# Kernel optimization log

Measured on AMD Instinct MI355X. Metric: run time of the kernel, lower is better.

## Reference

```python
import jax, jax.numpy as jnp
import numpy as np

B, S, H, E, V = 128, 128, 1024, 512, 32000

def setup_inputs() -> dict:
    key = jax.random.key(0)
    ks = jax.random.split(key, 14)
    sc = 0.02
    return {
        "x": jax.random.randint(ks[0], (B,), 0, V),
        "hidden": jax.random.normal(ks[1], (1, B, H), jnp.float32),
        "cell": jax.random.normal(ks[2], (1, B, H), jnp.float32),
        "encoder_outputs": jax.random.normal(ks[3], (B, S, H), jnp.float32),
        # parameters
        "emb_table": jax.random.normal(ks[4], (V, E), jnp.float32) * sc,
        "attn_W": jax.random.normal(ks[5], (H, 2 * H), jnp.float32) * sc,
        "attn_b": jnp.zeros((H,), jnp.float32),
        "v": jax.random.uniform(ks[6], (H,), jnp.float32),
        "W_ih": jax.random.normal(ks[7], (4 * H, E + H), jnp.float32) * sc,
        "W_hh": jax.random.normal(ks[8], (4 * H, H), jnp.float32) * sc,
        "b_ih": jnp.zeros((4 * H,), jnp.float32),
        "b_hh": jnp.zeros((4 * H,), jnp.float32),
        "fc_W": jax.random.normal(ks[9], (V, 2 * H), jnp.float32) * sc,
        "fc_b": jnp.zeros((V,), jnp.float32),
    }


def reference(x, hidden, cell, encoder_outputs, emb_table, attn_W, attn_b, v,
              W_ih, W_hh, b_ih, b_hh, fc_W, fc_b):
    b, s, h = encoder_outputs.shape
    h_last = hidden[-1]                      # [B,H]
    c_last = cell[-1]                        # [B,H]

    # Bahdanau attention
    h_rep = jnp.broadcast_to(h_last[:, None, :], (b, s, h))          # [B,S,H]
    cat = jnp.concatenate([h_rep, encoder_outputs], axis=2)          # [B,S,2H]
    energy = jnp.tanh(jnp.einsum('bsk,hk->bsh', cat, attn_W) + attn_b)
    score = jnp.einsum('bsh,h->bs', energy, v)                       # [B,S]
    attn_weights = jax.nn.softmax(score, axis=1)                     # [B,S]
    context = jnp.einsum('bs,bsh->bh', attn_weights, encoder_outputs)  # [B,H]

    # LSTM single step, gate order i,f,g,o (PyTorch convention)
    emb = emb_table[x]                                               # [B,E]
    xin = jnp.concatenate([emb, context], axis=1)                    # [B,E+H]
    gates = xin @ W_ih.T + b_ih + h_last @ W_hh.T + b_hh             # [B,4H]
    i, f, g, o = jnp.split(gates, 4, axis=1)
    c_new = jax.nn.sigmoid(f) * c_last + jax.nn.sigmoid(i) * jnp.tanh(g)
    h_new = jax.nn.sigmoid(o) * jnp.tanh(c_new)

    out = jnp.concatenate([h_new, context], axis=1)                  # [B,2H]
    logits = out @ fc_W.T + fc_b                                     # [B,V]
    return logits, h_new[None], c_new[None], attn_weights
```

## Files before the change

### kernel.cpp

```cpp
#include <hip/hip_runtime.h>
#include <hip/hip_bf16.h>
#include <math.h>

constexpr int B  = 128;
constexpr int S  = 128;
constexpr int H  = 1024;
constexpr int E  = 512;
constexpr int V  = 32000;
constexpr int H2 = 2 * H;
constexpr int G4 = 4 * H;
constexpr int KX = E + H;
constexpr int KG = KX + H;
constexpr int BS = B * S;
constexpr int KSPLIT = 4;
constexpr int KSEG = KG / KSPLIT;
constexpr int QSPLIT = 4;
constexpr int QSEG = H / QSPLIT;

typedef float  f32x4  __attribute__((ext_vector_type(4)));
typedef short  short8 __attribute__((ext_vector_type(8)));

#define VMCNT(N) asm volatile("s_waitcnt vmcnt(" #N ")" ::: "memory")
#define SBAR     asm volatile("s_barrier" ::: "memory")
#define SCHED0   __builtin_amdgcn_sched_barrier(0)

__device__ __forceinline__ short f2bf(float f) {
    union { float f; unsigned u; } x; x.f = f;
    unsigned r = (x.u + 0x7FFFu + ((x.u >> 16) & 1u)) >> 16;
    return (short)r;
}
__device__ __forceinline__ float bf2f(unsigned short u) {
    union { unsigned u; float f; } x; x.u = ((unsigned)u) << 16;
    return x.f;
}
__device__ __forceinline__ float fast_tanh(float x) {
    float z = fminf(fmaxf(x, -15.f), 15.f);
    float e = __expf(2.f * z);
    return 1.f - __fdividef(2.f, e + 1.f);
}
__device__ __forceinline__ short8 cvt8(float4 a, float4 b) {
    short8 r;
    r[0] = f2bf(a.x); r[1] = f2bf(a.y); r[2] = f2bf(a.z); r[3] = f2bf(a.w);
    r[4] = f2bf(b.x); r[5] = f2bf(b.y); r[6] = f2bf(b.z); r[7] = f2bf(b.w);
    return r;
}
__device__ __forceinline__ void glds16(const void* g, void* l) {
    __builtin_amdgcn_global_load_lds(
        (const __attribute__((address_space(1))) unsigned int*)g,
        (__attribute__((address_space(3))) unsigned int*)l,
        16, 0, 0);
}

__global__ __launch_bounds__(256) void k_pre(const float* __restrict__ enc,
                                             short* __restrict__ encb,
                                             const float* __restrict__ attn_W,
                                             short* __restrict__ w2b) {
    int bid = blockIdx.x;
    if (bid < 16384) {
        size_t p = (size_t)bid * 256 + threadIdx.x;
        float4 a = *(const float4*)(enc + p * 4);
        short4 o = { f2bf(a.x), f2bf(a.y), f2bf(a.z), f2bf(a.w) };
        *(short4*)(encb + p * 4) = o;
    } else {
        int p = (bid - 16384) * 256 + threadIdx.x;
        int row = p >> 8;
        int c = (p & 255) * 4;
        float4 a = *(const float4*)(attn_W + (size_t)row * H2 + H + c);
        short4 o = { f2bf(a.x), f2bf(a.y), f2bf(a.z), f2bf(a.w) };
        *(short4*)(w2b + (size_t)row * H + c) = o;
    }
}

__global__ __launch_bounds__(256) void k_q_mfma(const float* __restrict__ hlast,
                                                const float* __restrict__ attn_W,
                                                float* __restrict__ qpart) {
    __shared__ __align__(16) float A_s[2 * 4096];
    __shared__ __align__(16) float B_s[2 * 1024];

    const int tid  = threadIdx.x;
    const int wave = tid >> 6, lane = tid & 63;
    const int c16 = lane & 15, q4 = lane >> 4;
    const int n0 = blockIdx.x * 32;
    const int kbeg = blockIdx.y * QSEG;

    const int sc = ((lane & 7) ^ ((lane >> 3) & 7)) * 4;
    const int rA = (lane >> 3);
    const int rowB = wave * 8 + (lane >> 3);

    const float* gB = attn_W + (size_t)(n0 + rowB) * H2 + sc;

    auto stage = [&](int k0, int abo, int bbo) {
#pragma unroll
        for (int j = 0; j < 4; j++) {
            int row = wave * 32 + j * 8 + rA;
            glds16(hlast + (size_t)row * H + k0 + sc,
                   A_s + abo + wave * 1024 + j * 256);
        }
        glds16(gB + k0, B_s + bbo + wave * 256);
    };

    f32x4 acc[2][2] = {};
    stage(kbeg, 0, 0);

    for (int kk = 0; kk < QSEG / 32; kk++) {
        const int abo = (kk & 1) << 12;
        const int bbo = (kk & 1) << 10;
        if (kk < QSEG / 32 - 1) {
            stage(kbeg + (kk + 1) * 32, abo ^ 4096, bbo ^ 1024);
            VMCNT(5);
        } else {
            VMCNT(0);
        }
        SCHED0; SBAR;

        short8 a[2], bfr[2];
#pragma unroll
        for (int i = 0; i < 2; i++) {
            int ar = wave * 32 + i * 16 + c16;
            int cl = (2 * q4) ^ (ar & 7);
            float4 lo = *(const float4*)(A_s + abo + ar * 32 + cl * 4);
            float4 hi = *(const float4*)(A_s + abo + ar * 32 + (cl ^ 1) * 4);
            a[i] = cvt8(lo, hi);
        }
#pragma unroll
        for (int j = 0; j < 2; j++) {
            int rb = j * 16 + c16;
            int cl = (2 * q4) ^ (rb & 7);
            float4 lo = *(const float4*)(B_s + bbo + rb * 32 + cl * 4);
            float4 hi = *(const float4*)(B_s + bbo + rb * 32 + (cl ^ 1) * 4);
            bfr[j] = cvt8(lo, hi);
        }
#pragma unroll
        for (int i = 0; i < 2; i++)
#pragma unroll
            for (int j = 0; j < 2; j++)
                acc[i][j] = __builtin_amdgcn_mfma_f32_16x16x32_bf16(a[i], bfr[j], acc[i][j], 0, 0, 0);

        SCHED0; SBAR;
    }

    float* qp = qpart + (size_t)blockIdx.y * B * H;
#pragma unroll
    for (int i = 0; i < 2; i++)
#pragma unroll
        for (int j = 0; j < 2; j++)
#pragma unroll
            for (int r = 0; r < 4; r++) {
                int R = wave * 32 + i * 16 + q4 * 4 + r;
                int n = n0 + j * 16 + c16;
                qp[(size_t)R * H + n] = acc[i][j][r];
            }
}

__global__ __launch_bounds__(256) void k_energy_mfma(const short* __restrict__ encb,
                                                     const short* __restrict__ w2b,
                                                     const float* __restrict__ qpart,
                                                     const float* __restrict__ attn_b,
                                                     const float* __restrict__ v,
                                                     float* __restrict__ part) {
    __shared__ __align__(16) char smem[32768];
    short* Af = (short*)smem;
    short* Bf = (short*)(smem + 16384);
    float (*red)[33] = (float(*)[33])smem;

    const int tid  = threadIdx.x;
    const int wave = tid >> 6, lane = tid & 63;
    const int wr = wave >> 1, wc = wave & 1;
    const int c16 = lane & 15, q4 = lane >> 4;
    const int m0 = blockIdx.x * 128;
    const int n0 = blockIdx.y * 128;

    f32x4 acc[4][4] = {};

    const int scA   = ((lane & 3) ^ ((lane >> 3) & 3)) * 8;
    const int rowA0 = wave * 32 + (lane >> 2);
    const int rowA1 = rowA0 + 16;
    const int sa    = (c16 >> 1) & 3;

    const short* gA = encb + (size_t)m0 * H;
    const short* gB = w2b + (size_t)n0 * H;

    auto stage = [&](int k0, int dst) {
        glds16(gA + (size_t)rowA0 * H + k0 + scA, Af + dst + wave * 1024);
        glds16(gA + (size_t)rowA1 * H + k0 + scA, Af + dst + wave * 1024 + 512);
        glds16(gB + (size_t)rowA0 * H + k0 + scA, Bf + dst + wave * 1024);
        glds16(gB + (size_t)rowA1 * H + k0 + scA, Bf + dst + wave * 1024 + 512);
    };

    stage(0, 0);

    for (int kk = 0; kk < 32; kk++) {
        const int bo = (kk & 1) << 12;
        if (kk < 31) {
            stage((kk + 1) * 32, bo ^ 4096);
            VMCNT(4);
        } else {
            VMCNT(0);
        }
        SCHED0; SBAR;

        short8 a[4], b[4];
#pragma unroll
        for (int i = 0; i < 4; i++) {
            int r = wr * 64 + i * 16 + c16;
            a[i] = *(const short8*)(Af + bo + r * 32 + (q4 ^ sa) * 8);
        }
#pragma unroll
        for (int j = 0; j < 4; j++) {
            int r = wc * 64 + j * 16 + c16;
            b[j] = *(const short8*)(Bf + bo + r * 32 + (q4 ^ sa) * 8);
        }
#pragma unroll
        for (int i = 0; i < 4; i++)
#pragma unroll
            for (int j = 0; j < 4; j++)
                acc[i][j] = __builtin_amdgcn_mfma_f32_16x16x32_bf16(a[i], b[j], acc[i][j], 0, 0, 0);

        SCHED0; SBAR;
    }

    const int bb = blockIdx.x;
    float qv[4], vv[4];
#pragma unroll
    for (int j = 0; j < 4; j++) {
        int n = n0 + wc * 64 + j * 16 + c16;
        float s = attn_b[n];
#pragma unroll
        for (int kh = 0; kh < QSPLIT; kh++)
            s += qpart[((size_t)kh * B + bb) * H + n];
        qv[j] = s;
        vv[j] = v[n];
    }

#pragma unroll
    for (int i = 0; i < 4; i++) {
#pragma unroll
        for (int r = 0; r < 4; r++) {
            float s = 0.f;
#pragma unroll
            for (int j = 0; j < 4; j++)
                s += vv[j] * fast_tanh(qv[j] + acc[i][j][r]);
            red[wr * 64 + i * 16 + q4 * 4 + r][wc * 16 + c16] = s;
        }
    }
    __syncthreads();
    if (tid < 128) {
        float s = 0.f;
#pragma unroll
        for (int c = 0; c < 32; c++) s += red[tid][c];
        part[(size_t)(m0 + tid) * 8 + blockIdx.y] = s;
    }
}

__global__ __launch_bounds__(256) void k_softmax_ctx(const float* __restrict__ part,
                                                     const short* __restrict__ encb,
                                                     const int* __restrict__ x,
                                                     const float* __restrict__ emb,
                                                     const float* __restrict__ hlast,
                                                     float* __restrict__ attn_out,
                                                     short* __restrict__ xinb) {
    const int bid = blockIdx.x;
    const int b = bid >> 2, ch = bid & 3;
    const int tid = threadIdx.x;
    __shared__ float w[S];
    __shared__ float red[128];

    float val = 0.f;
    if (tid < S) {
        const float* p = part + (size_t)(b * S + tid) * 8;
#pragma unroll
        for (int t = 0; t < 8; t++) val += p[t];
        w[tid] = val;
        red[tid] = val;
    }
    __syncthreads();
#pragma unroll
    for (int s = 64; s > 0; s >>= 1) {
        if (tid < s) red[tid] = fmaxf(red[tid], red[tid + s]);
        __syncthreads();
    }
    float m = red[0];
    __syncthreads();
    if (tid < S) { val = __expf(w[tid] - m); red[tid] = val; }
    __syncthreads();
#pragma unroll
    for (int s = 64; s > 0; s >>= 1) {
        if (tid < s) red[tid] += red[tid + s];
        __syncthreads();
    }
    float inv = 1.f / red[0];
    if (tid < S) {
        val *= inv;
        w[tid] = val;
        if (ch == 0) attn_out[b * S + tid] = val;
    }
    if (ch == 1) {
        int xv = x[b];
        float2 e2 = *(const float2*)(emb + (size_t)xv * E + tid * 2);
        short2 eo = { f2bf(e2.x), f2bf(e2.y) };
        *(short2*)(xinb + (size_t)b * KG + tid * 2) = eo;
    } else if (ch == 2) {
        float4 h4 = *(const float4*)(hlast + (size_t)b * H + tid * 4);
        short4 ho = { f2bf(h4.x), f2bf(h4.y), f2bf(h4.z), f2bf(h4.w) };
        *(short4*)(xinb + (size_t)b * KG + KX + tid * 4) = ho;
    }
    __syncthreads();

    const int h = ch * 256 + tid;
    const unsigned short* e = (const unsigned short*)encb + (size_t)b * S * H + h;
    float a0 = 0.f;
#pragma unroll 8
    for (int s = 0; s < S; s++) a0 += w[s] * bf2f(e[(size_t)s * H]);
    xinb[(size_t)b * KG + E + h] = f2bf(a0);
}

__global__ __launch_bounds__(256) void k_gates_mfma(const short* __restrict__ xinb,
                                                    const float* __restrict__ W_ih,
                                                    const float* __restrict__ W_hh,
                                                    float* __restrict__ gpart) {
    __shared__ __align__(16) short A_s[2 * 4096];
    __shared__ __align__(16) float B_s[2 * 1024];

    const int tid  = threadIdx.x;
    const int wave = tid >> 6, lane = tid & 63;
    const int c16 = lane & 15, q4 = lane >> 4;
    const int n0 = blockIdx.x * 32;
    const int kbeg = blockIdx.y * KSEG;

    const int scA   = ((lane & 3) ^ ((lane >> 3) & 3)) * 8;
    const int rowA0 = wave * 32 + (lane >> 2);
    const int rowA1 = rowA0 + 16;
    const int rowB  = wave * 8 + (lane >> 3);
    const int scB   = ((lane & 7) ^ ((lane >> 3) & 7)) * 4;
    const int sa = (c16 >> 1) & 3;
    const int sb = c16 & 7;

    const short* gA0 = xinb + (size_t)rowA0 * KG + scA;
    const short* gA1 = xinb + (size_t)rowA1 * KG + scA;
    const int nr = n0 + rowB;

    auto bsrc = [&](int k0) -> const float* {
        return (k0 < KX) ? (W_ih + (size_t)nr * KX + k0 + scB)
                         : (W_hh + (size_t)nr * H + (k0 - KX) + scB);
    };
    auto stage = [&](int k0, int abo, int bbo) {
        glds16(gA0 + k0, A_s + abo + wave * 1024);
        glds16(gA1 + k0, A_s + abo + wave * 1024 + 512);
        glds16(bsrc(k0), B_s + bbo + wave * 256);
    };

    f32x4 acc[2][2] = {};
    stage(kbeg, 0, 0);

    for (int kk = 0; kk < KSEG / 32; kk++) {
        const int abo = (kk & 1) << 12;
        const int bbo = (kk & 1) << 10;
        if (kk < KSEG / 32 - 1) {
            stage(kbeg + (kk + 1) * 32, abo ^ 4096, bbo ^ 1024);
            VMCNT(3);
        } else {
            VMCNT(0);
        }
        SCHED0; SBAR;

        short8 a[2], bfr[2];
#pragma unroll
        for (int i = 0; i < 2; i++) {
            int r = wave * 32 + i * 16 + c16;
            a[i] = *(const short8*)(A_s + abo + r * 32 + (q4 ^ sa) * 8);
        }
#pragma unroll
        for (int j = 0; j < 2; j++) {
            int rb = j * 16 + c16;
            int cl = (2 * q4) ^ sb;
            float4 lo = *(const float4*)(B_s + bbo + rb * 32 + cl * 4);
            float4 hi = *(const float4*)(B_s + bbo + rb * 32 + (cl ^ 1) * 4);
            bfr[j] = cvt8(lo, hi);
        }
#pragma unroll
        for (int i = 0; i < 2; i++)
#pragma unroll
            for (int j = 0; j < 2; j++)
                acc[i][j] = __builtin_amdgcn_mfma_f32_16x16x32_bf16(a[i], bfr[j], acc[i][j], 0, 0, 0);

        SCHED0; SBAR;
    }

    float* gp = gpart + (size_t)blockIdx.y * B * G4;
#pragma unroll
    for (int i = 0; i < 2; i++)
#pragma unroll
        for (int j = 0; j < 2; j++)
#pragma unroll
            for (int r = 0; r < 4; r++) {
                int R = wave * 32 + i * 16 + q4 * 4 + r;
                int n = n0 + j * 16 + c16;
                gp[(size_t)R * G4 + n] = acc[i][j][r];
            }
}

__global__ __launch_bounds__(256) void k_lstm(const float* __restrict__ gpart,
                                              const float* __restrict__ cell,
                                              const float* __restrict__ b_ih,
                                              const float* __restrict__ b_hh,
                                              const short* __restrict__ xinb,
                                              float* __restrict__ out_h,
                                              float* __restrict__ out_c,
                                              short* __restrict__ xoutb) {
    int idx = blockIdx.x * 256 + threadIdx.x;
    int b = idx >> 10;
    int h = idx & (H - 1);
    float ig = b_ih[h]         + b_hh[h];
    float fg = b_ih[H + h]     + b_hh[H + h];
    float gg = b_ih[2 * H + h] + b_hh[2 * H + h];
    float og = b_ih[3 * H + h] + b_hh[3 * H + h];
#pragma unroll
    for (int p = 0; p < KSPLIT; p++) {
        const float* g = gpart + ((size_t)p * B + b) * G4;
        ig += g[h]; fg += g[H + h]; gg += g[2 * H + h]; og += g[3 * H + h];
    }
    float si = 1.f / (1.f + expf(-ig));
    float sf = 1.f / (1.f + expf(-fg));
    float so = 1.f / (1.f + expf(-og));
    float c = sf * cell[idx] + si * tanhf(gg);
    float hn = so * tanhf(c);
    out_h[idx] = hn;
    out_c[idx] = c;
    xoutb[(size_t)b * H2 + h] = f2bf(hn);
    xoutb[(size_t)b * H2 + H + h] = xinb[(size_t)b * KG + E + h];
}

__global__ __launch_bounds__(256) void k_fc_mfma(const short* __restrict__ xoutb,
                                                 const float* __restrict__ fcW,
                                                 const float* __restrict__ fcb,
                                                 float* __restrict__ logits) {
    __shared__ __align__(16) short A_s[2 * 4096];
    __shared__ __align__(16) float B_s[2 * 1024];

    const int tid  = threadIdx.x;
    const int wave = tid >> 6, lane = tid & 63;
    const int c16 = lane & 15, q4 = lane >> 4;
    const int n0 = blockIdx.x * 32;

    const int scA   = ((lane & 3) ^ ((lane >> 3) & 3)) * 8;
    const int rowA0 = wave * 32 + (lane >> 2);
    const int rowA1 = rowA0 + 16;
    const int rowB  = wave * 8 + (lane >> 3);
    const int scB   = ((lane & 7) ^ ((lane >> 3) & 7)) * 4;
    const int sa = (c16 >> 1) & 3;
    const int sb = c16 & 7;

    const short* gA0 = xoutb + (size_t)rowA0 * H2 + scA;
    const short* gA1 = xoutb + (size_t)rowA1 * H2 + scA;
    const float* gBr = fcW + (size_t)(n0 + rowB) * H2 + scB;

    auto stage = [&](int k0, int abo, int bbo) {
        glds16(gA0 + k0, A_s + abo + wave * 1024);
        glds16(gA1 + k0, A_s + abo + wave * 1024 + 512);
        glds16(gBr + k0, B_s + bbo + wave * 256);
    };

    f32x4 acc[2][2] = {};
    stage(0, 0, 0);

    for (int kk = 0; kk < H2 / 32; kk++) {
        const int abo = (kk & 1) << 12;
        const int bbo = (kk & 1) << 10;
        if (kk < H2 / 32 - 1) {
            stage((kk + 1) * 32, abo ^ 4096, bbo ^ 1024);
            VMCNT(3);
        } else {
            VMCNT(0);
        }
        SCHED0; SBAR;

        short8 a[2], bfr[2];
#pragma unroll
        for (int i = 0; i < 2; i++) {
            int r = wave * 32 + i * 16 + c16;
            a[i] = *(const short8*)(A_s + abo + r * 32 + (q4 ^ sa) * 8);
        }
#pragma unroll
        for (int j = 0; j < 2; j++) {
            int rb = j * 16 + c16;
            int cl = (2 * q4) ^ sb;
            float4 lo = *(const float4*)(B_s + bbo + rb * 32 + cl * 4);
            float4 hi = *(const float4*)(B_s + bbo + rb * 32 + (cl ^ 1) * 4);
            bfr[j] = cvt8(lo, hi);
        }
#pragma unroll
        for (int i = 0; i < 2; i++)
#pragma unroll
            for (int j = 0; j < 2; j++)
                acc[i][j] = __builtin_amdgcn_mfma_f32_16x16x32_bf16(a[i], bfr[j], acc[i][j], 0, 0, 0);

        SCHED0; SBAR;
    }

#pragma unroll
    for (int i = 0; i < 2; i++)
#pragma unroll
        for (int j = 0; j < 2; j++) {
            int n = n0 + j * 16 + c16;
            float bias = fcb[n];
#pragma unroll
            for (int r = 0; r < 4; r++) {
                int R = wave * 32 + i * 16 + q4 * 4 + r;
                logits[(size_t)R * V + n] = acc[i][j][r] + bias;
            }
        }
}

extern "C" void kernel_launch(void* const* d_in, const int* in_sizes, int n_in,
                              void* d_out, int out_size, void* d_ws, size_t ws_size,
                              hipStream_t stream) {
    const int*   x      = (const int*)d_in[0];
    const float* hidden = (const float*)d_in[1];
    const float* cell   = (const float*)d_in[2];
    const float* enc    = (const float*)d_in[3];
    const float* emb    = (const float*)d_in[4];
    const float* attn_W = (const float*)d_in[5];
    const float* attn_b = (const float*)d_in[6];
    const float* v      = (const float*)d_in[7];
    const float* W_ih   = (const float*)d_in[8];
    const float* W_hh   = (const float*)d_in[9];
    const float* b_ih   = (const float*)d_in[10];
    const float* b_hh   = (const float*)d_in[11];
    const float* fc_W   = (const float*)d_in[12];
    const float* fc_b   = (const float*)d_in[13];

    float* out = (float*)d_out;
    float* logits   = out;
    float* out_h    = out + (size_t)B * V;
    float* out_c    = out_h + (size_t)B * H;
    float* out_attn = out_c + (size_t)B * H;

    char* ws = (char*)d_ws;
    short* encb  = (short*)ws;   ws += (size_t)BS * H * 2;
    short* w2b   = (short*)ws;   ws += (size_t)H * H * 2;
    short* xinb  = (short*)ws;   ws += (size_t)B * KG * 2;
    short* xoutb = (short*)ws;   ws += (size_t)B * H2 * 2;
    float* qpart = (float*)ws;   ws += (size_t)QSPLIT * B * H * 4;
    float* part  = (float*)ws;   ws += (size_t)BS * 8 * 4;
    float* gpart = (float*)ws;   ws += (size_t)KSPLIT * B * G4 * 4;

    k_q_mfma<<<dim3(H / 32, QSPLIT), dim3(256), 0, stream>>>(hidden, attn_W, qpart);
    k_pre<<<dim3(16384 + 1024), dim3(256), 0, stream>>>(enc, encb, attn_W, w2b);
    k_energy_mfma<<<dim3(BS / 128, H / 128), dim3(256), 0, stream>>>(encb, w2b, qpart,
                                                                     attn_b, v, part);
    k_softmax_ctx<<<dim3(B * 4), dim3(256), 0, stream>>>(part, encb, x, emb, hidden, out_attn, xinb);
    k_gates_mfma<<<dim3(G4 / 32, KSPLIT), dim3(256), 0, stream>>>(xinb, W_ih, W_hh, gpart);
    k_lstm<<<dim3(B * H / 256), dim3(256), 0, stream>>>(gpart, cell, b_ih, b_hh, xinb,
                                                        out_h, out_c, xoutb);
    k_fc_mfma<<<dim3(V / 32), dim3(256), 0, stream>>>(xoutb, fc_W, fc_b, logits);
}
```

Measured before the change: 580.9 us.

## Deepen global-to-LDS prefetch pipelines and drop second barrier per iteration

The energy GEMM moves from two to three LDS buffers with prefetch distance 2, and the gates and fc GEMMs move to four buffers with prefetch distance 3. Every main loop now uses a single barrier per iteration, placed before the next stage is issued, so the trailing barrier that protected buffer reuse can go. The q projection loop instead waits for all loads each iteration before prefetching, which shortens its overlap. This is meant to hide global load latency in the memory-bound weight-streaming GEMMs, at the cost of more LDS per block and possibly lower occupancy.

```diff
diff --git a/kernel.cpp b/kernel.cpp
--- a/kernel.cpp
+++ b/kernel.cpp
@@ -89,30 +89,26 @@
 
     const float* gB = attn_W + (size_t)(n0 + rowB) * H2 + sc;
 
-    auto stage = [&](int k0, int abo, int bbo) {
+    auto stage = [&](int k0, int buf) {
 #pragma unroll
         for (int j = 0; j < 4; j++) {
             int row = wave * 32 + j * 8 + rA;
             glds16(hlast + (size_t)row * H + k0 + sc,
-                   A_s + abo + wave * 1024 + j * 256);
-        }
-        glds16(gB + k0, B_s + bbo + wave * 256);
+                   A_s + buf * 4096 + wave * 1024 + j * 256);
+        }
+        glds16(gB + k0, B_s + buf * 1024 + wave * 256);
     };
 
     f32x4 acc[2][2] = {};
-    stage(kbeg, 0, 0);
+    stage(kbeg, 0);
 
     for (int kk = 0; kk < QSEG / 32; kk++) {
+        VMCNT(0);
+        SCHED0; SBAR; SCHED0;
+        if (kk + 1 < QSEG / 32) stage(kbeg + (kk + 1) * 32, (kk + 1) & 1);
+
         const int abo = (kk & 1) << 12;
         const int bbo = (kk & 1) << 10;
-        if (kk < QSEG / 32 - 1) {
-            stage(kbeg + (kk + 1) * 32, abo ^ 4096, bbo ^ 1024);
-            VMCNT(5);
-        } else {
-            VMCNT(0);
-        }
-        SCHED0; SBAR;
-
         short8 a[2], bfr[2];
 #pragma unroll
         for (int i = 0; i < 2; i++) {
@@ -135,8 +131,6 @@
 #pragma unroll
             for (int j = 0; j < 2; j++)
                 acc[i][j] = __builtin_amdgcn_mfma_f32_16x16x32_bf16(a[i], bfr[j], acc[i][j], 0, 0, 0);
-
-        SCHED0; SBAR;
     }
 
     float* qp = qpart + (size_t)blockIdx.y * B * H;
@@ -158,9 +152,9 @@
                                                      const float* __restrict__ attn_b,
                                                      const float* __restrict__ v,
                                                      float* __restrict__ part) {
-    __shared__ __align__(16) char smem[32768];
+    __shared__ __align__(16) char smem[49152];
     short* Af = (short*)smem;
-    short* Bf = (short*)(smem + 16384);
+    short* Bf = (short*)(smem + 24576);
     float (*red)[33] = (float(*)[33])smem;
 
     const int tid  = threadIdx.x;
@@ -180,25 +174,22 @@
     const short* gA = encb + (size_t)m0 * H;
     const short* gB = w2b + (size_t)n0 * H;
 
-    auto stage = [&](int k0, int dst) {
-        glds16(gA + (size_t)rowA0 * H + k0 + scA, Af + dst + wave * 1024);
-        glds16(gA + (size_t)rowA1 * H + k0 + scA, Af + dst + wave * 1024 + 512);
-        glds16(gB + (size_t)rowA0 * H + k0 + scA, Bf + dst + wave * 1024);
-        glds16(gB + (size_t)rowA1 * H + k0 + scA, Bf + dst + wave * 1024 + 512);
+    auto stage = [&](int k0, int buf) {
+        glds16(gA + (size_t)rowA0 * H + k0 + scA, Af + buf * 4096 + wave * 1024);
+        glds16(gA + (size_t)rowA1 * H + k0 + scA, Af + buf * 4096 + wave * 1024 + 512);
+        glds16(gB + (size_t)rowA0 * H + k0 + scA, Bf + buf * 4096 + wave * 1024);
+        glds16(gB + (size_t)rowA1 * H + k0 + scA, Bf + buf * 4096 + wave * 1024 + 512);
     };
 
     stage(0, 0);
+    stage(32, 1);
 
     for (int kk = 0; kk < 32; kk++) {
-        const int bo = (kk & 1) << 12;
-        if (kk < 31) {
-            stage((kk + 1) * 32, bo ^ 4096);
-            VMCNT(4);
-        } else {
-            VMCNT(0);
-        }
-        SCHED0; SBAR;
-
+        if (kk < 31) { VMCNT(4); } else { VMCNT(0); }
+        SCHED0; SBAR; SCHED0;
+        if (kk + 2 < 32) stage((kk + 2) * 32, (kk + 2) % 3);
+
+        const int bo = (kk % 3) * 4096;
         short8 a[4], b[4];
 #pragma unroll
         for (int i = 0; i < 4; i++) {
@@ -215,9 +206,8 @@
 #pragma unroll
             for (int j = 0; j < 4; j++)
                 acc[i][j] = __builtin_amdgcn_mfma_f32_16x16x32_bf16(a[i], b[j], acc[i][j], 0, 0, 0);
-
-        SCHED0; SBAR;
-    }
+    }
+    __syncthreads();
 
     const int bb = blockIdx.x;
     float qv[4], vv[4];
@@ -318,14 +308,15 @@
                                                     const float* __restrict__ W_ih,
                                                     const float* __restrict__ W_hh,
                                                     float* __restrict__ gpart) {
-    __shared__ __align__(16) short A_s[2 * 4096];
-    __shared__ __align__(16) float B_s[2 * 1024];
+    __shared__ __align__(16) short A_s[4 * 4096];
+    __shared__ __align__(16) float B_s[4 * 1024];
 
     const int tid  = threadIdx.x;
     const int wave = tid >> 6, lane = tid & 63;
     const int c16 = lane & 15, q4 = lane >> 4;
     const int n0 = blockIdx.x * 32;
     const int kbeg = blockIdx.y * KSEG;
+    constexpr int NIT = KSEG / 32;
 
     const int scA   = ((lane & 3) ^ ((lane >> 3) & 3)) * 8;
     const int rowA0 = wave * 32 + (lane >> 2);
@@ -343,26 +334,26 @@
         return (k0 < KX) ? (W_ih + (size_t)nr * KX + k0 + scB)
                          : (W_hh + (size_t)nr * H + (k0 - KX) + scB);
     };
-    auto stage = [&](int k0, int abo, int bbo) {
-        glds16(gA0 + k0, A_s + abo + wave * 1024);
-        glds16(gA1 + k0, A_s + abo + wave * 1024 + 512);
-        glds16(bsrc(k0), B_s + bbo + wave * 256);
+    auto stage = [&](int k0, int buf) {
+        glds16(gA0 + k0, A_s + buf * 4096 + wave * 1024);
+        glds16(gA1 + k0, A_s + buf * 4096 + wave * 1024 + 512);
+        glds16(bsrc(k0), B_s + buf * 1024 + wave * 256);
     };
 
     f32x4 acc[2][2] = {};
-    stage(kbeg, 0, 0);
-
-    for (int kk = 0; kk < KSEG / 32; kk++) {
-        const int abo = (kk & 1) << 12;
-        const int bbo = (kk & 1) << 10;
-        if (kk < KSEG / 32 - 1) {
-            stage(kbeg + (kk + 1) * 32, abo ^ 4096, bbo ^ 1024);
-            VMCNT(3);
-        } else {
-            VMCNT(0);
-        }
-        SCHED0; SBAR;
-
+    stage(kbeg, 0);
+    stage(kbeg + 32, 1);
+    stage(kbeg + 64, 2);
+
+    for (int kk = 0; kk < NIT; kk++) {
+        if (kk < NIT - 2)      { VMCNT(6); }
+        else if (kk == NIT - 2){ VMCNT(3); }
+        else                   { VMCNT(0); }
+        SCHED0; SBAR; SCHED0;
+        if (kk + 3 < NIT) stage(kbeg + (kk + 3) * 32, (kk + 3) & 3);
+
+        const int abo = (kk & 3) << 12;
+        const int bbo = (kk & 3) << 10;
         short8 a[2], bfr[2];
 #pragma unroll
         for (int i = 0; i < 2; i++) {
@@ -382,8 +373,6 @@
 #pragma unroll
             for (int j = 0; j < 2; j++)
                 acc[i][j] = __builtin_amdgcn_mfma_f32_16x16x32_bf16(a[i], bfr[j], acc[i][j], 0, 0, 0);
-
-        SCHED0; SBAR;
     }
 
     float* gp = gpart + (size_t)blockIdx.y * B * G4;
@@ -434,13 +423,14 @@
                                                  const float* __restrict__ fcW,
                                                  const float* __restrict__ fcb,
                                                  float* __restrict__ logits) {
-    __shared__ __align__(16) short A_s[2 * 4096];
-    __shared__ __align__(16) float B_s[2 * 1024];
+    __shared__ __align__(16) short A_s[4 * 4096];
+    __shared__ __align__(16) float B_s[4 * 1024];
 
     const int tid  = threadIdx.x;
     const int wave = tid >> 6, lane = tid & 63;
     const int c16 = lane & 15, q4 = lane >> 4;
     const int n0 = blockIdx.x * 32;
+    constexpr int NIT = H2 / 32;
 
     const int scA   = ((lane & 3) ^ ((lane >> 3) & 3)) * 8;
     const int rowA0 = wave * 32 + (lane >> 2);
@@ -454,26 +444,26 @@
     const short* gA1 = xoutb + (size_t)rowA1 * H2 + scA;
     const float* gBr = fcW + (size_t)(n0 + rowB) * H2 + scB;
 
-    auto stage = [&](int k0, int abo, int bbo) {
-        glds16(gA0 + k0, A_s + abo + wave * 1024);
-        glds16(gA1 + k0, A_s + abo + wave * 1024 + 512);
-        glds16(gBr + k0, B_s + bbo + wave * 256);
+    auto stage = [&](int k0, int buf) {
+        glds16(gA0 + k0, A_s + buf * 4096 + wave * 1024);
+        glds16(gA1 + k0, A_s + buf * 4096 + wave * 1024 + 512);
+        glds16(gBr + k0, B_s + buf * 1024 + wave * 256);
     };
 
     f32x4 acc[2][2] = {};
-    stage(0, 0, 0);
-
-    for (int kk = 0; kk < H2 / 32; kk++) {
-        const int abo = (kk & 1) << 12;
-        const int bbo = (kk & 1) << 10;
-        if (kk < H2 / 32 - 1) {
-            stage((kk + 1) * 32, abo ^ 4096, bbo ^ 1024);
-            VMCNT(3);
-        } else {
-            VMCNT(0);
-        }
-        SCHED0; SBAR;
-
+    stage(0, 0);
+    stage(32, 1);
+    stage(64, 2);
+
+    for (int kk = 0; kk < NIT; kk++) {
+        if (kk < NIT - 2)      { VMCNT(6); }
+        else if (kk == NIT - 2){ VMCNT(3); }
+        else                   { VMCNT(0); }
+        SCHED0; SBAR; SCHED0;
+        if (kk + 3 < NIT) stage((kk + 3) * 32, (kk + 3) & 3);
+
+        const int abo = (kk & 3) << 12;
+        const int bbo = (kk & 3) << 10;
         short8 a[2], bfr[2];
 #pragma unroll
         for (int i = 0; i < 2; i++) {
@@ -493,8 +483,6 @@
 #pragma unroll
             for (int j = 0; j < 2; j++)
                 acc[i][j] = __builtin_amdgcn_mfma_f32_16x16x32_bf16(a[i], bfr[j], acc[i][j], 0, 0, 0);
-
-        SCHED0; SBAR;
     }
 
 #pragma unroll
```

Result: slower. 619.9 us (+6.7%).
